# Performance work log

Hardware: AMD Instinct MI355X
Metric: run time of the kernel (lower is better)

Reference implementation:

```python
import jax, jax.numpy as jnp
import numpy as np

B, S, D = 2, 2048, 1280
H = 20
HD = D // H  # 64, rotary dim


def setup_inputs() -> dict:
    key = jax.random.key(0)
    ks = jax.random.split(key, 4)
    scale = 0.02
    return {
        "hidden_states": jax.random.normal(ks[0], (B, S, D), jnp.float32),
        "Wq": jax.random.normal(ks[1], (D, D), jnp.float32) * scale,
        "bq": jnp.zeros((D,), jnp.float32),
        "Wk": jax.random.normal(ks[2], (D, D), jnp.float32) * scale,
        "bk": jnp.zeros((D,), jnp.float32),
        "Wv": jax.random.normal(ks[3], (D, D), jnp.float32) * scale,
        "bv": jnp.zeros((D,), jnp.float32),
    }


def _rotate_half(x):
    x1, x2 = jnp.split(x, 2, axis=-1)
    return jnp.concatenate((-x2, x1), axis=-1)


def _rotary_cos_sin(seq_len, dim, dtype):
    inv_freq = 1.0 / (10000.0 ** (jnp.arange(0, dim, 2, dtype=jnp.float32) / dim))
    t = jnp.arange(seq_len, dtype=jnp.float32)
    freqs = jnp.einsum("i,j->ij", t, inv_freq)          # [S, dim/2]
    emb = jnp.concatenate((freqs, freqs), axis=-1)        # [S, dim]
    return jnp.cos(emb).astype(dtype)[None, None], jnp.sin(emb).astype(dtype)[None, None]


def reference(hidden_states, Wq, bq, Wk, bk, Wv, bv):
    b, s, d = hidden_states.shape
    # QKV projections, split heads -> [B, H, S, HD]
    def proj(W, bias):
        y = hidden_states @ W + bias
        return y.reshape(b, s, H, HD).transpose(0, 2, 1, 3)

    q = proj(Wq, bq) * (HD ** -0.5)  # scale BEFORE rotary, as in source
    k = proj(Wk, bk)
    v = proj(Wv, bv)

    cos, sin = _rotary_cos_sin(s, HD, q.dtype)
    q = q * cos + _rotate_half(q) * sin
    k = k * cos + _rotate_half(k) * sin

    scores = jnp.einsum("bhqd,bhkd->bhqk", q, k)
    probs = jax.nn.softmax(scores, axis=-1)
    ctx = jnp.einsum("bhqk,bhkd->bhqd", probs, v)
    return ctx.transpose(0, 2, 1, 3).reshape(b, s, d)
```

## Files before the change

kernel.cpp:

```cpp
#include <hip/hip_runtime.h>

#define DD 1280
#define SS 2048
#define HH 20

typedef __bf16 bf16x8 __attribute__((ext_vector_type(8)));
typedef float f32x4 __attribute__((ext_vector_type(4)));

typedef __attribute__((address_space(3))) unsigned int lds_uint;
typedef __attribute__((address_space(1))) unsigned int glb_uint;
#define GLL16(g, l) __builtin_amdgcn_global_load_lds((const glb_uint*)(g), (lds_uint*)(l), 16, 0, 0)

__device__ __forceinline__ unsigned short f2bf(float f) {
  union { float f; unsigned u; } v; v.f = f;
  unsigned r = v.u + 0x7fffu + ((v.u >> 16) & 1u);
  return (unsigned short)(r >> 16);
}
__device__ __forceinline__ unsigned f2u(float f) {
  union { float f; unsigned u; } v; v.f = f; return v.u;
}
__device__ __forceinline__ unsigned pk2(float lo, float hi) {
  return ((unsigned)f2bf(hi) << 16) | (unsigned)f2bf(lo);
}

__global__ __launch_bounds__(256) void prep_kernel(
    const float* __restrict__ X, const float* __restrict__ Wq,
    const float* __restrict__ Wk, const float* __restrict__ Wv,
    unsigned short* __restrict__ Xb, unsigned short* __restrict__ WT,
    float2* __restrict__ cs) {
  __shared__ __align__(8) unsigned short tile[64][68];
  int bid = blockIdx.x, tid = threadIdx.x;
  if (bid < 320) {
#pragma unroll
    for (int it = 0; it < 8; it++) {
      size_t base = (size_t)(it * 320 + bid) * 2048 + (size_t)tid * 8;
      const float4* xin = (const float4*)(X + base);
      float4 a = xin[0], c = xin[1];
      uint4 o = make_uint4(pk2(a.x, a.y), pk2(a.z, a.w), pk2(c.x, c.y), pk2(c.z, c.w));
      *(uint4*)(Xb + base) = o;
    }
  } else if (bid < 1520) {
    int wb = bid - 320;
    int mat = wb / 400;
    int t = wb % 400;
    int tn = t % 20, tk = t / 20;
    const float* W = (mat == 0) ? Wq : ((mat == 1) ? Wk : Wv);
    int k0 = tk * 64, n0 = tn * 64;
    int r = tid >> 2, cq = tid & 3;
    const float* src = W + (size_t)(k0 + r) * DD + n0 + cq * 16;
#pragma unroll
    for (int j = 0; j < 4; j++) {
      float4 wv = *(const float4*)(src + j * 4);
      *(ushort4*)&tile[r][cq * 16 + j * 4] =
          make_ushort4(f2bf(wv.x), f2bf(wv.y), f2bf(wv.z), f2bf(wv.w));
    }
    __syncthreads();
    unsigned short* out = WT + (size_t)mat * DD * DD + (size_t)(n0 + r) * DD + k0 + cq * 16;
#pragma unroll
    for (int j = 0; j < 4; j++) {
      ushort4 o = make_ushort4(tile[cq * 16 + j * 4 + 0][r], tile[cq * 16 + j * 4 + 1][r],
                               tile[cq * 16 + j * 4 + 2][r], tile[cq * 16 + j * 4 + 3][r]);
      *(ushort4*)(out + j * 4) = o;
    }
  } else {
#pragma unroll
    for (int it = 0; it < 4; it++) {
      int idx = (bid - 1520) * 1024 + it * 256 + tid;
      int sp = idx >> 5, j = idx & 31;
      float invf = exp2f(-(float)j * 0.41524101186092034f);
      float ang = (float)sp * invf;
      cs[idx] = make_float2(cosf(ang), sinf(ang));
    }
  }
}

__global__ __launch_bounds__(256) void qkv_gemm_kernel(
    const unsigned short* __restrict__ Xb, const unsigned short* __restrict__ WT,
    const float* __restrict__ bq, const float* __restrict__ bk, const float* __restrict__ bv,
    const float2* __restrict__ cs,
    unsigned short* __restrict__ Qr, unsigned short* __restrict__ Kr,
    unsigned short* __restrict__ VT) {
  __shared__ __align__(16) unsigned short As[128 * 32];
  __shared__ __align__(16) unsigned short Bs[128 * 32];
  int bx0 = blockIdx.x;
  int bx = (bx0 & 7) * 120 + (bx0 >> 3);
  int mat = bx / 320;
  int r0 = bx % 320;
  int tm = r0 / 10, tn = r0 % 10;
  int m0 = tm * 128, n0 = tn * 128;
  int tid = threadIdx.x;
  int lane = tid & 63, wave = tid >> 6;
  int c15 = lane & 15, quad = lane >> 4;
  int wm = wave >> 1, wn = wave & 1;
  const unsigned short* Wm = WT + (size_t)mat * DD * DD;

  int rowA = tid >> 2;
  int c8 = (tid & 3) * 8;
  const unsigned short* gA0 = Xb + (size_t)(m0 + rowA) * DD + c8;
  const unsigned short* gA1 = gA0 + (size_t)64 * DD;
  const unsigned short* gB0 = Wm + (size_t)(n0 + rowA) * DD + c8;
  const unsigned short* gB1 = gB0 + (size_t)64 * DD;
  unsigned short* ldsA0 = As + wave * 512;
  unsigned short* ldsA1 = As + 2048 + wave * 512;
  unsigned short* ldsB0 = Bs + wave * 512;
  unsigned short* ldsB1 = Bs + 2048 + wave * 512;

  f32x4 acc[4][4] = {};

  for (int kk = 0; kk < DD; kk += 32) {
    __syncthreads();
    GLL16(gA0 + kk, ldsA0);
    GLL16(gA1 + kk, ldsA1);
    GLL16(gB0 + kk, ldsB0);
    GLL16(gB1 + kk, ldsB1);
    __syncthreads();
    bf16x8 af[4];
#pragma unroll
    for (int mi = 0; mi < 4; mi++)
      af[mi] = *(const bf16x8*)(As + (wm * 64 + mi * 16 + c15) * 32 + quad * 8);
#pragma unroll
    for (int ni = 0; ni < 4; ni++) {
      bf16x8 bfr = *(const bf16x8*)(Bs + (wn * 64 + ni * 16 + c15) * 32 + quad * 8);
#pragma unroll
      for (int mi = 0; mi < 4; mi++)
        acc[mi][ni] = __builtin_amdgcn_mfma_f32_16x16x32_bf16(af[mi], bfr, acc[mi][ni], 0, 0, 0);
    }
  }

  int growb = m0 + wm * 64;
  int gcolb = n0 + wn * 64;
  if (mat == 2) {
#pragma unroll
    for (int mi = 0; mi < 4; mi++) {
      int row0 = growb + mi * 16 + quad * 4;
      int bb_ = row0 >> 11, sp = row0 & 2047;
#pragma unroll
      for (int ni = 0; ni < 4; ni++) {
        int gcol = gcolb + ni * 16 + c15;
        float bias = bv[gcol];
        int hh = gcol >> 6, dd = gcol & 63;
        f32x4 v = acc[mi][ni];
        ushort4 o = make_ushort4(f2bf(v[0] + bias), f2bf(v[1] + bias),
                                 f2bf(v[2] + bias), f2bf(v[3] + bias));
        *(ushort4*)(VT + ((size_t)((bb_ * HH + hh) * 64 + dd)) * SS + sp) = o;
      }
    }
  } else {
    unsigned short* Out = (mat == 0) ? Qr : Kr;
    const float* bias = (mat == 0) ? bq : bk;
    float qs = (mat == 0) ? 0.18033688011112042f : 1.0f;
#pragma unroll
    for (int mi = 0; mi < 4; mi++) {
      int row0 = growb + mi * 16 + quad * 4;
#pragma unroll
      for (int ni = 0; ni < 2; ni++) {
        int gcol_lo = gcolb + ni * 16 + c15;
        int gcol_hi = gcol_lo + 32;
        float blo = bias[gcol_lo], bhi = bias[gcol_hi];
        int d = ni * 16 + c15;
        f32x4 lo = acc[mi][ni], hi = acc[mi][ni + 2];
#pragma unroll
        for (int r = 0; r < 4; r++) {
          int grow = row0 + r;
          float2 cv = cs[(size_t)(grow & 2047) * 32 + d];
          float xl = (lo[r] + blo) * qs, xh = (hi[r] + bhi) * qs;
          Out[(size_t)grow * DD + gcol_lo] = f2bf(xl * cv.x - xh * cv.y);
          Out[(size_t)grow * DD + gcol_hi] = f2bf(xh * cv.x + xl * cv.y);
        }
      }
    }
  }
}

__global__ __launch_bounds__(256)
void attn_kernel(
    const unsigned short* __restrict__ Qr, const unsigned short* __restrict__ Kr,
    const unsigned short* __restrict__ VT, float* __restrict__ out) {
  __shared__ __align__(16) unsigned short Klds[3][2048];
  __shared__ __align__(16) unsigned short Vlds[3][2048];
  __shared__ __align__(16) unsigned short Pall[4][512];
  int bx = blockIdx.x;
  int bh = bx % 40, qt = bx / 40;
  int b = bh / HH, h = bh % HH;
  int tid = threadIdx.x;
  int lane = tid & 63, w = tid >> 6;
  int c15 = lane & 15, quad = lane >> 4;
  int q0 = qt * 64 + w * 16;

  const unsigned short* Qb = Qr + (size_t)(b * SS + q0 + c15) * DD + h * 64 + quad * 8;
  bf16x8 qf[2];
  qf[0] = *(const bf16x8*)(Qb);
  qf[1] = *(const bf16x8*)(Qb + 32);

  int krow = tid >> 3, kch = tid & 7;
  const unsigned short* Ksrc = Kr + (size_t)(b * SS + krow) * DD + h * 64
                               + ((kch ^ (krow & 7)) * 8);
  int vrow = tid >> 2, vch = tid & 3;
  const unsigned short* Vsrc = VT + (size_t)(bh * 64 + vrow) * SS
                               + ((vch ^ ((vrow >> 1) & 3)) * 8);
  unsigned short* Pw = &Pall[w][0];

  bf16x8 ones;
#pragma unroll
  for (int i = 0; i < 8; i++) ones[i] = (__bf16)1.0f;

  f32x4 of[4] = {};
  f32x4 ol = {};

  GLL16(Ksrc,                    &Klds[0][0] + w * 512);
  GLL16(Vsrc,                    &Vlds[0][0] + w * 512);
  GLL16(Ksrc + (size_t)32 * DD,  &Klds[1][0] + w * 512);
  GLL16(Vsrc + 32,               &Vlds[1][0] + w * 512);
  asm volatile("s_waitcnt vmcnt(2)" ::: "memory");
  __builtin_amdgcn_sched_barrier(0);
  __builtin_amdgcn_s_barrier();

  for (int t = 0; t < 64; t++) {
    int cur = t % 3;
    if (t + 2 < 64) {
      int nxt = (t + 2) % 3;
      GLL16(Ksrc + (size_t)((t + 2) * 32) * DD, &Klds[nxt][0] + w * 512);
      GLL16(Vsrc + (t + 2) * 32,                &Vlds[nxt][0] + w * 512);
    }
    const unsigned short* Kb = &Klds[cur][0];
    const unsigned short* Vb = &Vlds[cur][0];

    f32x4 sc[2] = {};
#pragma unroll
    for (int kc = 0; kc < 2; kc++)
#pragma unroll
      for (int ni = 0; ni < 2; ni++) {
        int R = ni * 16 + c15;
        bf16x8 kf = *(const bf16x8*)(Kb + R * 64 + (((kc * 4 + quad) ^ (R & 7)) * 8));
        sc[ni] = __builtin_amdgcn_mfma_f32_16x16x32_bf16(qf[kc], kf, sc[ni], 0, 0, 0);
      }

#pragma unroll
    for (int ni = 0; ni < 2; ni++)
#pragma unroll
      for (int r = 0; r < 4; r++) {
        unsigned u = f2u(__builtin_amdgcn_exp2f(sc[ni][r]));
        int q = quad * 4 + r;
        int sw = (ni * 2 + (c15 >> 3)) ^ ((q >> 1) & 3);
        Pw[q * 32 + sw * 8 + (c15 & 7)] = (unsigned short)(u >> 16);
      }

    bf16x8 pf = *(const bf16x8*)(Pw + c15 * 32 + ((quad ^ ((c15 >> 1) & 3)) * 8));
#pragma unroll
    for (int nio = 0; nio < 4; nio++) {
      int R = nio * 16 + c15;
      bf16x8 vf = *(const bf16x8*)(Vb + R * 32 + ((quad ^ ((R >> 1) & 3)) * 8));
      of[nio] = __builtin_amdgcn_mfma_f32_16x16x32_bf16(pf, vf, of[nio], 0, 0, 0);
    }
    ol = __builtin_amdgcn_mfma_f32_16x16x32_bf16(pf, ones, ol, 0, 0, 0);

    if (t + 2 < 64) {
      asm volatile("s_waitcnt vmcnt(2)" ::: "memory");
    } else {
      asm volatile("s_waitcnt vmcnt(0)" ::: "memory");
    }
    __builtin_amdgcn_sched_barrier(0);
    __builtin_amdgcn_s_barrier();
  }

#pragma unroll
  for (int r = 0; r < 4; r++) {
    float invl = 1.0f / ol[r];
    float* op = out + (size_t)(b * SS + q0 + quad * 4 + r) * DD + h * 64 + c15;
#pragma unroll
    for (int nio = 0; nio < 4; nio++)
      op[nio * 16] = of[nio][r] * invl;
  }
}

extern "C" void kernel_launch(void* const* d_in, const int* in_sizes, int n_in,
                              void* d_out, int out_size, void* d_ws, size_t ws_size,
                              hipStream_t stream) {
  (void)in_sizes; (void)n_in; (void)out_size; (void)ws_size;
  const float* X  = (const float*)d_in[0];
  const float* Wq = (const float*)d_in[1];
  const float* bq = (const float*)d_in[2];
  const float* Wk = (const float*)d_in[3];
  const float* bk = (const float*)d_in[4];
  const float* Wv = (const float*)d_in[5];
  const float* bv = (const float*)d_in[6];
  char* ws = (char*)d_ws;
  unsigned short* Xb  = (unsigned short*)(ws);
  unsigned short* WT  = (unsigned short*)(ws + 10485760);
  unsigned short* Qr  = (unsigned short*)(ws + 20316160);
  unsigned short* Kr  = (unsigned short*)(ws + 30801920);
  unsigned short* VTt = (unsigned short*)(ws + 41287680);
  float2* cstab       = (float2*)(ws + 51773440);
  hipLaunchKernelGGL(prep_kernel, dim3(1584), dim3(256), 0, stream, X, Wq, Wk, Wv, Xb, WT, cstab);
  hipLaunchKernelGGL(qkv_gemm_kernel, dim3(960), dim3(256), 0, stream, Xb, WT, bq, bk, bv, cstab, Qr, Kr, VTt);
  hipLaunchKernelGGL(attn_kernel, dim3(1280), dim3(256), 0, stream, Qr, Kr, VTt, (float*)d_out);
}
```

Baseline: 228.3 us.

## Compute transposed scores to feed P directly from registers, drop LDS round trip

Swaps the QK^T MFMA operand order so each lane holds scores for one query across its own keys. This lets the exponentiated probabilities be packed straight into the bf16 A-operand of the PV MFMA, with no write to and re-read from shared memory. The row sum is now accumulated in scalar registers and reduced with lane shuffles at the end, replacing the extra MFMA against a vector of ones. V fragments are gathered as two 8-byte loads so the key ordering matches the new P layout; this removes LDS traffic and one MFMA per tile, at the cost of narrower V loads.

```diff
diff --git a/kernel.cpp b/kernel.cpp
--- a/kernel.cpp
+++ b/kernel.cpp
@@ -18,6 +18,9 @@
 }
 __device__ __forceinline__ unsigned f2u(float f) {
   union { float f; unsigned u; } v; v.f = f; return v.u;
+}
+__device__ __forceinline__ float u2f(unsigned x) {
+  union { unsigned u; float f; } v; v.u = x; return v.f;
 }
 __device__ __forceinline__ unsigned pk2(float lo, float hi) {
   return ((unsigned)f2bf(hi) << 16) | (unsigned)f2bf(lo);
@@ -178,7 +181,6 @@
     const unsigned short* __restrict__ VT, float* __restrict__ out) {
   __shared__ __align__(16) unsigned short Klds[3][2048];
   __shared__ __align__(16) unsigned short Vlds[3][2048];
-  __shared__ __align__(16) unsigned short Pall[4][512];
   int bx = blockIdx.x;
   int bh = bx % 40, qt = bx / 40;
   int b = bh / HH, h = bh % HH;
@@ -198,14 +200,9 @@
   int vrow = tid >> 2, vch = tid & 3;
   const unsigned short* Vsrc = VT + (size_t)(bh * 64 + vrow) * SS
                                + ((vch ^ ((vrow >> 1) & 3)) * 8);
-  unsigned short* Pw = &Pall[w][0];
-
-  bf16x8 ones;
-#pragma unroll
-  for (int i = 0; i < 8; i++) ones[i] = (__bf16)1.0f;
 
   f32x4 of[4] = {};
-  f32x4 ol = {};
+  float ol = 0.f;
 
   GLL16(Ksrc,                    &Klds[0][0] + w * 512);
   GLL16(Vsrc,                    &Vlds[0][0] + w * 512);
@@ -232,27 +229,39 @@
       for (int ni = 0; ni < 2; ni++) {
         int R = ni * 16 + c15;
         bf16x8 kf = *(const bf16x8*)(Kb + R * 64 + (((kc * 4 + quad) ^ (R & 7)) * 8));
-        sc[ni] = __builtin_amdgcn_mfma_f32_16x16x32_bf16(qf[kc], kf, sc[ni], 0, 0, 0);
+        sc[ni] = __builtin_amdgcn_mfma_f32_16x16x32_bf16(kf, qf[kc], sc[ni], 0, 0, 0);
       }
 
-#pragma unroll
-    for (int ni = 0; ni < 2; ni++)
-#pragma unroll
-      for (int r = 0; r < 4; r++) {
-        unsigned u = f2u(__builtin_amdgcn_exp2f(sc[ni][r]));
-        int q = quad * 4 + r;
-        int sw = (ni * 2 + (c15 >> 3)) ^ ((q >> 1) & 3);
-        Pw[q * 32 + sw * 8 + (c15 & 7)] = (unsigned short)(u >> 16);
-      }
-
-    bf16x8 pf = *(const bf16x8*)(Pw + c15 * 32 + ((quad ^ ((c15 >> 1) & 3)) * 8));
+    unsigned e0 = f2u(__builtin_amdgcn_exp2f(sc[0][0]));
+    unsigned e1 = f2u(__builtin_amdgcn_exp2f(sc[0][1]));
+    unsigned e2 = f2u(__builtin_amdgcn_exp2f(sc[0][2]));
+    unsigned e3 = f2u(__builtin_amdgcn_exp2f(sc[0][3]));
+    unsigned e4 = f2u(__builtin_amdgcn_exp2f(sc[1][0]));
+    unsigned e5 = f2u(__builtin_amdgcn_exp2f(sc[1][1]));
+    unsigned e6 = f2u(__builtin_amdgcn_exp2f(sc[1][2]));
+    unsigned e7 = f2u(__builtin_amdgcn_exp2f(sc[1][3]));
+    union { unsigned u[4]; bf16x8 v; } af;
+    af.u[0] = (e1 & 0xffff0000u) | (e0 >> 16);
+    af.u[1] = (e3 & 0xffff0000u) | (e2 >> 16);
+    af.u[2] = (e5 & 0xffff0000u) | (e4 >> 16);
+    af.u[3] = (e7 & 0xffff0000u) | (e6 >> 16);
+    {
+      float s01 = u2f(e0 & 0xffff0000u) + u2f(e1 & 0xffff0000u);
+      float s23 = u2f(e2 & 0xffff0000u) + u2f(e3 & 0xffff0000u);
+      float s45 = u2f(e4 & 0xffff0000u) + u2f(e5 & 0xffff0000u);
+      float s67 = u2f(e6 & 0xffff0000u) + u2f(e7 & 0xffff0000u);
+      ol += (s01 + s23) + (s45 + s67);
+    }
+
 #pragma unroll
     for (int nio = 0; nio < 4; nio++) {
       int R = nio * 16 + c15;
-      bf16x8 vf = *(const bf16x8*)(Vb + R * 32 + ((quad ^ ((R >> 1) & 3)) * 8));
-      of[nio] = __builtin_amdgcn_mfma_f32_16x16x32_bf16(pf, vf, of[nio], 0, 0, 0);
-    }
-    ol = __builtin_amdgcn_mfma_f32_16x16x32_bf16(pf, ones, ol, 0, 0, 0);
+      int f = (R >> 1) & 3;
+      union { ushort4 s[2]; bf16x8 v; } vf;
+      vf.s[0] = *(const ushort4*)(Vb + R * 32 + ((((quad >> 1)) ^ f) * 8) + (quad & 1) * 4);
+      vf.s[1] = *(const ushort4*)(Vb + R * 32 + (((2 + (quad >> 1)) ^ f) * 8) + (quad & 1) * 4);
+      of[nio] = __builtin_amdgcn_mfma_f32_16x16x32_bf16(af.v, vf.v, of[nio], 0, 0, 0);
+    }
 
     if (t + 2 < 64) {
       asm volatile("s_waitcnt vmcnt(2)" ::: "memory");
@@ -263,9 +272,14 @@
     __builtin_amdgcn_s_barrier();
   }
 
+  float lt = ol;
+  lt += __shfl_xor(lt, 16);
+  lt += __shfl_xor(lt, 32);
+
 #pragma unroll
   for (int r = 0; r < 4; r++) {
-    float invl = 1.0f / ol[r];
+    float lq = __shfl(lt, quad * 4 + r);
+    float invl = 1.0f / lq;
     float* op = out + (size_t)(b * SS + q0 + quad * 4 + r) * DD + h * 64 + c15;
 #pragma unroll
     for (int nio = 0; nio < 4; nio++)
```

After: 227.4 us. About the same (-0.4%).
